# Performance work log

Measured on AMD Instinct MI355X. Metric: run time of the kernel, lower is better.

## Reference

```python
import jax, jax.numpy as jnp
import numpy as np
from jax import lax

NUM_CLASSES = 20
NUM_ANCHORS = 5
COORDS = 4
NMS_TH = 0.45
PRE_TH = 0.005
FEAT_STRIDE = 32.0
BIASES = jnp.array([[1.08, 1.19], [3.42, 4.41], [6.63, 11.38],
                    [9.42, 5.11], [16.62, 10.52]], dtype=jnp.float32)  # [A,2]


def setup_inputs() -> dict:
    key = jax.random.key(0)
    B, H, W = 16, 26, 26
    C = (NUM_CLASSES + COORDS + 1) * NUM_ANCHORS  # 125
    x = jax.random.normal(key, (B, C, H, W), dtype=jnp.float32)
    im_info = jnp.array([480.0, 640.0], dtype=jnp.float32)  # (orig_h, orig_w)
    return {"x": x, "im_info": im_info}


def _pairwise_iou(b):
    # b: [N,4] center-format (cx, cy, w, h)
    x1 = b[:, 0] - b[:, 2] * 0.5
    y1 = b[:, 1] - b[:, 3] * 0.5
    x2 = b[:, 0] + b[:, 2] * 0.5
    y2 = b[:, 1] + b[:, 3] * 0.5
    area = (x2 - x1) * (y2 - y1)
    iw = jnp.maximum(jnp.minimum(x2[:, None], x2[None, :]) - jnp.maximum(x1[:, None], x1[None, :]), 0.0)
    ih = jnp.maximum(jnp.minimum(y2[:, None], y2[None, :]) - jnp.maximum(y1[:, None], y1[None, :]), 0.0)
    inter = iw * ih
    return inter / (area[:, None] + area[None, :] - inter + 1e-12)


def _nms_scores(boxes, scores):
    # greedy single-class NMS; returns scores with pre-threshold + suppressed boxes zeroed
    N = scores.shape[0]
    s = jnp.where(scores < PRE_TH, 0.0, scores)
    order = jnp.argsort(-s)
    ss = s[order]
    iou = lax.stop_gradient(_pairwise_iou(boxes[order]))  # [N,N]
    idx = jnp.arange(N)

    def body(i, keep):
        ki = keep[i] & (ss[i] > 0.0)
        sup = ki & (iou[i] > NMS_TH) & (idx > i)
        return keep & (~sup)

    keep_sorted = lax.fori_loop(0, N, body, jnp.ones((N,), dtype=bool))
    keep = jnp.zeros((N,), dtype=bool).at[order].set(keep_sorted)
    return jnp.where(keep, s, 0.0)


def _forward(x, im_info):
    B, C, H, W = x.shape
    A = NUM_ANCHORS
    fdt = x.dtype

    # --- Slice + activations (channel layout per SLICE_POINTS [10,20,25,125]) ---
    xy = jax.nn.sigmoid(x[:, :2 * A]).reshape(B, A, 2, H, W)
    wh = x[:, 2 * A:4 * A].reshape(B, A, 2, H, W)
    obj = jax.nn.sigmoid(x[:, 4 * A:5 * A])                    # [B,A,H,W]
    conf = x[:, 5 * A:].reshape(B, NUM_CLASSES, A, H, W)

    # --- class probability (plain softmax over class axis 1) + top predictions ---
    class_prob = jax.nn.softmax(conf, axis=1)                  # [B,C,A,H,W]
    top = class_prob * obj[:, None]                            # scale by objectness
    preds = jnp.concatenate([top, obj[:, None]], axis=1)       # [B,C+1,A,H,W]

    # --- YoloBBs: decode boxes on the grid, darknet correct_region_boxes ---
    col = jnp.arange(W, dtype=fdt)[None, None, None, :]
    row = jnp.arange(H, dtype=fdt)[None, None, :, None]
    bx = (col + xy[:, :, 0]) / W                               # [B,A,H,W]
    by = (row + xy[:, :, 1]) / H
    bw = BIASES[None, :, 0, None, None] * jnp.exp(wh[:, :, 0]) / W
    bh = BIASES[None, :, 1, None, None] * jnp.exp(wh[:, :, 1]) / H

    netw = W * FEAT_STRIDE
    neth = H * FEAT_STRIDE
    im_h, im_w = im_info[0], im_info[1]
    cond = (netw / im_w) < (neth / im_h)
    new_w = jnp.where(cond, netw, im_w * neth / im_h)
    new_h = jnp.where(cond, im_h * netw / im_w, neth)
    bx = (bx - (netw - new_w) * 0.5 / netw) / (new_w / netw)
    by = (by - (neth - new_h) * 0.5 / neth) / (new_h / neth)
    bw = bw * (netw / new_w)
    bh = bh * (neth / new_h)
    bboxs = jnp.stack([bx * im_w, by * im_h, bw * im_w, bh * im_h], axis=-1)
    N = A * H * W
    bboxs = bboxs.reshape(B, N, 4)                             # [B,N,4] (cx,cy,w,h) pixels

    # --- NMSFilter (classes=1, first_class=NUM_CLASSES -> objectness channel) ---
    preds_flat = preds.reshape(B, NUM_CLASSES + 1, N)
    obj_scores = preds_flat[:, NUM_CLASSES]                    # [B,N]
    new_obj = jax.vmap(_nms_scores)(bboxs, obj_scores)
    preds_flat = preds_flat.at[:, NUM_CLASSES].set(new_obj)

    # --- YoloEvalCompat: class axis moved last ---
    prob = jnp.transpose(preds_flat, (0, 2, 1))                # [B,N,C+1]
    return prob, bboxs


def reference(x, im_info):
    return _forward(x, im_info)
```

## Files before the change

kernel.cpp:

```cpp
#include <hip/hip_runtime.h>
#include <stdint.h>

#pragma clang fp contract(off)

#define NCLS   20
#define NA     5
#define NB     16
#define Hg     26
#define Wg     26
#define HWc    (Hg*Wg)
#define NBOX   (NA*HWc)
#define NPAD   4096
#define NWRD   (NPAD/64)
#define NROW   3392
#define SWRD   53
#define PROBC  (NCLS+1)
#define PRE_TH 0.005f
#define NMS_TH 0.45f
#define ECHUNK 1024
#define ETOT   88192
#define SEGB(c) (32*(c)*((c)-1))

__constant__ float c_bias[10] = {1.08f,1.19f,3.42f,4.41f,6.63f,11.38f,9.42f,5.11f,16.62f,10.52f};

__global__ __launch_bounds__(256) void k_decode(const float* __restrict__ x,
                                                const float* __restrict__ im_info,
                                                float* __restrict__ out,
                                                float* __restrict__ scores) {
  int t = blockIdx.x * 256 + threadIdx.x;
  if (t >= NB * NBOX) return;
  int b  = t / NBOX;
  int n  = t - b * NBOX;
  int a  = n / HWc;
  int hw = n - a * HWc;
  int h  = hw / Wg;
  int w  = hw - h * Wg;

  const float* xb = x + (size_t)b * 125 * HWc;
  float tx = xb[(2*a  ) * HWc + hw];
  float ty = xb[(2*a+1) * HWc + hw];
  float tw = xb[(10+2*a) * HWc + hw];
  float th = xb[(11+2*a) * HWc + hw];
  float to = xb[(20+a  ) * HWc + hw];

  float sx  = 1.0f / (1.0f + expf(-tx));
  float sy  = 1.0f / (1.0f + expf(-ty));
  float obj = 1.0f / (1.0f + expf(-to));

  float cf[NCLS];
  float mx = -3.402823e38f;
#pragma unroll
  for (int c = 0; c < NCLS; ++c) {
    cf[c] = xb[(25 + c*NA + a) * HWc + hw];
    mx = fmaxf(mx, cf[c]);
  }
  float sum = 0.f;
#pragma unroll
  for (int c = 0; c < NCLS; ++c) { cf[c] = expf(cf[c] - mx); sum += cf[c]; }

  float* op = out + ((size_t)b * NBOX + n) * PROBC;
#pragma unroll
  for (int c = 0; c < NCLS; ++c) op[c] = cf[c] / sum * obj;
  op[NCLS] = 0.f;

  float Wf = (float)Wg, Hf = (float)Hg;
  float bx = ((float)w + sx) / Wf;
  float by = ((float)h + sy) / Hf;
  float bw = c_bias[2*a]   * expf(tw) / Wf;
  float bh = c_bias[2*a+1] * expf(th) / Hf;
  float netw = Wf * 32.0f;
  float neth = Hf * 32.0f;
  float imh = im_info[0], imw = im_info[1];
  bool cond   = (netw / imw) < (neth / imh);
  float new_w = cond ? netw : (imw * neth / imh);
  float new_h = cond ? (imh * netw / imw) : neth;
  bx = (bx - (netw - new_w) * 0.5f / netw) / (new_w / netw);
  by = (by - (neth - new_h) * 0.5f / neth) / (new_h / neth);
  bw = bw * (netw / new_w);
  bh = bh * (neth / new_h);
  float X  = bx * imw, Y = by * imh, Wd = bw * imw, Hd = bh * imh;

  float* ob = out + (size_t)NB * NBOX * PROBC + ((size_t)b * NBOX + n) * 4;
  ob[0] = X; ob[1] = Y; ob[2] = Wd; ob[3] = Hd;

  scores[t] = (obj < PRE_TH) ? 0.f : obj;
}

__global__ __launch_bounds__(1024) void k_sort(const float* __restrict__ scores,
                                               const float* __restrict__ out,
                                               float* __restrict__ sScore,
                                               int* __restrict__ sIdx,
                                               float4* __restrict__ sBox,
                                               unsigned long long* __restrict__ posm,
                                               int* __restrict__ cnt) {
  int b    = blockIdx.x;
  int tid  = threadIdx.x;
  int lane = tid & 63;
  int wv   = tid >> 6;
  __shared__ unsigned long long key[NPAD];

  if (tid < SWRD) cnt[b * SWRD + tid] = 0;

  for (int i = tid; i < NPAD; i += 1024) {
    unsigned long long k = 0ULL;
    if (i < NBOX) {
      float s = scores[b * NBOX + i];
      unsigned int bits = __float_as_uint(s);
      k = ((unsigned long long)bits << 32) | (unsigned long long)(0xFFFFFFFFu - (unsigned)i);
    }
    key[i] = k;
  }
  __syncthreads();

  for (int k = 2; k <= 256; k <<= 1) {
    for (int j = k >> 1; j > 0; j >>= 1) {
#pragma unroll
      for (int qq = 0; qq < 2; ++qq) {
        int q  = lane + (qq << 6);
        int li = ((q & ~(j - 1)) << 1) | (q & (j - 1));
        int i  = (wv << 8) + li;
        int ix = i | j;
        bool desc = ((i & k) == 0);
        unsigned long long a = key[i], c = key[ix];
        bool sw = desc ? (a < c) : (a > c);
        if (sw) { key[i] = c; key[ix] = a; }
      }
      asm volatile("" ::: "memory");
    }
  }
  __syncthreads();

  for (int k = 512; k <= NPAD; k <<= 1) {
    for (int j = k >> 1; j >= 256; j >>= 1) {
#pragma unroll
      for (int qq = 0; qq < 2; ++qq) {
        int q  = tid + (qq << 10);
        int i  = ((q & ~(j - 1)) << 1) | (q & (j - 1));
        int ix = i | j;
        bool desc = ((i & k) == 0);
        unsigned long long a = key[i], c = key[ix];
        bool sw = desc ? (a < c) : (a > c);
        if (sw) { key[i] = c; key[ix] = a; }
      }
      __syncthreads();
    }
    {
      bool desc = (((wv << 8) & k) == 0);
      for (int j = 128; j > 0; j >>= 1) {
#pragma unroll
        for (int qq = 0; qq < 2; ++qq) {
          int q  = lane + (qq << 6);
          int li = ((q & ~(j - 1)) << 1) | (q & (j - 1));
          int i  = (wv << 8) + li;
          int ix = i | j;
          unsigned long long a = key[i], c = key[ix];
          bool sw = desc ? (a < c) : (a > c);
          if (sw) { key[i] = c; key[ix] = a; }
        }
        asm volatile("" ::: "memory");
      }
      __syncthreads();
    }
  }

  const float4* outBox = (const float4*)(out + (size_t)NB * NBOX * PROBC);
  for (int i = tid; i < NPAD; i += 1024) {
    unsigned long long k = key[i];
    float s = __uint_as_float((unsigned)(k >> 32));
    bool pos = (k >> 32) != 0ULL;
    unsigned long long bal = __ballot(pos);
    if ((tid & 63) == 0) posm[b * NWRD + (i >> 6)] = bal;
    sScore[b * NPAD + i] = s;
    int oi = (int)(0xFFFFFFFFu - (unsigned)(k & 0xFFFFFFFFu));
    sIdx[b * NPAD + i] = oi;
    float4 bx = make_float4(0.f, 0.f, 0.f, 0.f);
    if (oi >= 0 && oi < NBOX) bx = outBox[(size_t)b * NBOX + oi];
    sBox[b * NPAD + i] = bx;
  }
}

__global__ __launch_bounds__(64) void k_supmat(const float4* __restrict__ sBox,
                                               unsigned long long* __restrict__ diag,
                                               ulonglong2* __restrict__ entries,
                                               int* __restrict__ cnt) {
  int colg = blockIdx.x;
  int rowg = blockIdx.y;
  if (colg < rowg) return;
  int b = blockIdx.z;
  int l = threadIdx.x;

  __shared__ float4 corn[64];
  __shared__ float  car[64];

  float4 cb = sBox[(size_t)b * NPAD + colg * 64 + l];
  float c1 = cb.x - cb.z * 0.5f;
  float d1 = cb.y - cb.w * 0.5f;
  float c2 = cb.x + cb.z * 0.5f;
  float d2 = cb.y + cb.w * 0.5f;
  corn[l] = make_float4(c1, d1, c2, d2);
  car[l]  = (c2 - c1) * (d2 - d1);
  __syncthreads();

  int row = rowg * 64 + l;
  float4 rb = sBox[(size_t)b * NPAD + row];
  float bx1 = rb.x - rb.z * 0.5f;
  float by1 = rb.y - rb.w * 0.5f;
  float bx2 = rb.x + rb.z * 0.5f;
  float by2 = rb.y + rb.w * 0.5f;
  float areai = (bx2 - bx1) * (by2 - by1);

  int jmin = row - colg * 64;
  unsigned long long bits = 0ULL;
#pragma unroll 4
  for (int t2 = 0; t2 < 64; ++t2) {
    float4 cc = corn[t2];
    float aj  = car[t2];
    float iw = fminf(bx2, cc.z) - fmaxf(bx1, cc.x); iw = fmaxf(iw, 0.0f);
    float ih = fminf(by2, cc.w) - fmaxf(by1, cc.y); ih = fmaxf(ih, 0.0f);
    float inter = iw * ih;
    bool sup = inter > NMS_TH * (areai + aj - inter + 1e-12f);
    if (sup & (t2 > jmin)) bits |= 1ULL << t2;
  }

  if (colg == rowg) {
    diag[((size_t)b * SWRD + colg) * 64 + l] = bits;
  } else if (bits) {
    int p = atomicAdd(&cnt[b * SWRD + colg], 1);
    entries[(size_t)b * ETOT + SEGB(colg) + p] =
        ulonglong2{(unsigned long long)row, bits};
  }
}

__global__ __launch_bounds__(512) void k_scan(const unsigned long long* __restrict__ diag,
                                              const ulonglong2* __restrict__ entries,
                                              const int* __restrict__ cnt,
                                              const unsigned long long* __restrict__ posm,
                                              const float* __restrict__ sScore,
                                              const int* __restrict__ sIdx,
                                              float* __restrict__ out) {
  int b    = blockIdx.x;
  int tid  = threadIdx.x;
  int lane = tid & 63;
  int wid  = tid >> 6;
  __shared__ unsigned long long diagS[SWRD * 64];
  __shared__ ulonglong2 ebuf[2][ECHUNK];
  __shared__ unsigned long long remv[SWRD];
  __shared__ int cntS[SWRD];

  const ulonglong2* segB = entries + (size_t)b * ETOT;

  if (tid < SWRD) {
    remv[tid] = ~posm[b * NWRD + tid];
    cntS[tid] = cnt[b * SWRD + tid];
  }
  for (int i = tid; i < SWRD * 64; i += 512)
    diagS[i] = diag[(size_t)b * SWRD * 64 + i];
  __syncthreads();

  for (int c = 0; c < SWRD; ++c) {
    if (wid > 0) {
      if (c + 1 < SWRD) {
        int nn = cntS[c + 1];
        if (nn > ECHUNK) nn = ECHUNK;
        const ulonglong2* sp = segB + SEGB(c + 1);
        for (int g = tid - 64; g < nn; g += 448) ebuf[(c + 1) & 1][g] = sp[g];
      }
    } else {
      int nc = cntS[c];
      int nl = nc > ECHUNK ? ECHUNK : nc;
      unsigned long long acc = 0ULL;
      for (int g = lane; g < nl; g += 64) {
        ulonglong2 e = ebuf[c & 1][g];
        int row = (int)e.x;
        if (!((remv[row >> 6] >> (row & 63)) & 1ULL)) acc |= e.y;
      }
      for (int g = ECHUNK + lane; g < nc; g += 64) {
        ulonglong2 e = segB[SEGB(c) + g];
        int row = (int)e.x;
        if (!((remv[row >> 6] >> (row & 63)) & 1ULL)) acc |= e.y;
      }
#pragma unroll
      for (int off = 32; off >= 1; off >>= 1) acc |= __shfl_xor(acc, off);

      unsigned long long cur = remv[c] | acc;
      unsigned long long dg  = diagS[(c << 6) + lane];
      unsigned long long m   = __ballot(dg != 0ULL);
      while (m) {
        int k = __ffsll((long long)m) - 1;
        m &= m - 1;
        unsigned long long dk = __shfl(dg, k);
        if (!((cur >> k) & 1ULL)) cur |= dk;
      }
      if (lane == 0) remv[c] = cur;
    }
    __syncthreads();
  }

  for (int p = tid; p < NBOX; p += 512) {
    if (!((remv[p >> 6] >> (p & 63)) & 1ULL)) {
      int oi  = sIdx[b * NPAD + p];
      float s = sScore[b * NPAD + p];
      out[((size_t)b * NBOX + oi) * PROBC + NCLS] = s;
    }
  }
}

extern "C" void kernel_launch(void* const* d_in, const int* in_sizes, int n_in,
                              void* d_out, int out_size, void* d_ws, size_t ws_size,
                              hipStream_t stream) {
  const float* x  = (const float*)d_in[0];
  const float* im = (const float*)d_in[1];
  float* out = (float*)d_out;

  float* scores = (float*)d_ws;
  float* sScore = scores + (size_t)NB * NBOX;
  int*   sIdx   = (int*)(sScore + (size_t)NB * NPAD);
  float4* sBox  = (float4*)(sIdx + (size_t)NB * NPAD);
  unsigned long long* posm = (unsigned long long*)(sBox + (size_t)NB * NPAD);
  unsigned long long* diag = posm + (size_t)NB * NWRD;
  int* cnt = (int*)(diag + (size_t)NB * SWRD * 64);
  ulonglong2* entries = (ulonglong2*)((char*)cnt + (((size_t)NB * SWRD * 4 + 15) & ~(size_t)15));

  hipLaunchKernelGGL(k_decode, dim3((NB * NBOX + 255) / 256), dim3(256), 0, stream,
                     x, im, out, scores);
  hipLaunchKernelGGL(k_sort, dim3(NB), dim3(1024), 0, stream,
                     scores, out, sScore, sIdx, sBox, posm, cnt);
  hipLaunchKernelGGL(k_supmat, dim3(SWRD, SWRD, NB), dim3(64), 0, stream,
                     sBox, diag, entries, cnt);
  hipLaunchKernelGGL(k_scan, dim3(NB), dim3(512), 0, stream,
                     diag, entries, cnt, posm, sScore, sIdx, out);
}
```

Baseline: 209.4 us.

## Preload all suppression entries into LDS once, removing per-column syncs

Measured after the change: 249.1 us. +18.9%, slower.

```diff
diff --git a/kernel.cpp b/kernel.cpp
--- a/kernel.cpp
+++ b/kernel.cpp
@@ -17,9 +17,10 @@
 #define PROBC  (NCLS+1)
 #define PRE_TH 0.005f
 #define NMS_TH 0.45f
-#define ECHUNK 1024
+#define ECAP   8192
 #define ETOT   88192
 #define SEGB(c) (32*(c)*((c)-1))
+#define DYNLDS ((SWRD*64 + ECAP) * 8 + ECAP * 2)
 
 __constant__ float c_bias[10] = {1.08f,1.19f,3.42f,4.41f,6.63f,11.38f,9.42f,5.11f,16.62f,10.52f};
 
@@ -242,42 +243,61 @@
   int tid  = threadIdx.x;
   int lane = tid & 63;
   int wid  = tid >> 6;
-  __shared__ unsigned long long diagS[SWRD * 64];
-  __shared__ ulonglong2 ebuf[2][ECHUNK];
+
+  extern __shared__ char dynS[];
+  unsigned long long* diagS = (unsigned long long*)dynS;
+  unsigned long long* bitsS = diagS + SWRD * 64;
+  unsigned short*     rowS  = (unsigned short*)(bitsS + ECAP);
   __shared__ unsigned long long remv[SWRD];
-  __shared__ int cntS[SWRD];
+  __shared__ int offs[SWRD + 1];
 
   const ulonglong2* segB = entries + (size_t)b * ETOT;
 
-  if (tid < SWRD) {
-    remv[tid] = ~posm[b * NWRD + tid];
-    cntS[tid] = cnt[b * SWRD + tid];
-  }
+  if (tid < SWRD) remv[tid] = ~posm[b * NWRD + tid];
   for (int i = tid; i < SWRD * 64; i += 512)
     diagS[i] = diag[(size_t)b * SWRD * 64 + i];
-  __syncthreads();
-
-  for (int c = 0; c < SWRD; ++c) {
-    if (wid > 0) {
-      if (c + 1 < SWRD) {
-        int nn = cntS[c + 1];
-        if (nn > ECHUNK) nn = ECHUNK;
-        const ulonglong2* sp = segB + SEGB(c + 1);
-        for (int g = tid - 64; g < nn; g += 448) ebuf[(c + 1) & 1][g] = sp[g];
-      }
-    } else {
-      int nc = cntS[c];
-      int nl = nc > ECHUNK ? ECHUNK : nc;
+
+  if (wid == 0) {
+    int v = (lane < SWRD) ? cnt[b * SWRD + lane] : 0;
+    int s = v;
+#pragma unroll
+    for (int d = 1; d < 64; d <<= 1) {
+      int o = __shfl_up(s, d);
+      if (lane >= d) s += o;
+    }
+    if (lane < SWRD) offs[lane + 1] = s;
+    if (lane == 0)  offs[0] = 0;
+  }
+  __syncthreads();
+
+  int total = offs[SWRD];
+  bool inLds = (total <= ECAP);
+  if (inLds) {
+    for (int g = tid; g < total; g += 512) {
+      int lo = 0, hi = SWRD;
+      while (hi - lo > 1) { int mid = (lo + hi) >> 1; if (offs[mid] <= g) lo = mid; else hi = mid; }
+      ulonglong2 e = segB[SEGB(lo) + (g - offs[lo])];
+      bitsS[g] = e.y;
+      rowS[g]  = (unsigned short)e.x;
+    }
+  }
+  __syncthreads();
+
+  if (wid == 0) {
+    for (int c = 0; c < SWRD; ++c) {
+      int e0 = offs[c], e1 = offs[c + 1];
       unsigned long long acc = 0ULL;
-      for (int g = lane; g < nl; g += 64) {
-        ulonglong2 e = ebuf[c & 1][g];
-        int row = (int)e.x;
-        if (!((remv[row >> 6] >> (row & 63)) & 1ULL)) acc |= e.y;
-      }
-      for (int g = ECHUNK + lane; g < nc; g += 64) {
-        ulonglong2 e = segB[SEGB(c) + g];
-        int row = (int)e.x;
-        if (!((remv[row >> 6] >> (row & 63)) & 1ULL)) acc |= e.y;
+      if (inLds) {
+        for (int g = e0 + lane; g < e1; g += 64) {
+          int row = rowS[g];
+          if (!((remv[row >> 6] >> (row & 63)) & 1ULL)) acc |= bitsS[g];
+        }
+      } else {
+        for (int g = e0 + lane; g < e1; g += 64) {
+          ulonglong2 e = segB[SEGB(c) + (g - e0)];
+          int row = (int)e.x;
+          if (!((remv[row >> 6] >> (row & 63)) & 1ULL)) acc |= e.y;
+        }
       }
 #pragma unroll
       for (int off = 32; off >= 1; off >>= 1) acc |= __shfl_xor(acc, off);
@@ -293,8 +313,8 @@
       }
       if (lane == 0) remv[c] = cur;
     }
-    __syncthreads();
-  }
+  }
+  __syncthreads();
 
   for (int p = tid; p < NBOX; p += 512) {
     if (!((remv[p >> 6] >> (p & 63)) & 1ULL)) {
@@ -321,12 +341,19 @@
   int* cnt = (int*)(diag + (size_t)NB * SWRD * 64);
   ulonglong2* entries = (ulonglong2*)((char*)cnt + (((size_t)NB * SWRD * 4 + 15) & ~(size_t)15));
 
+  static bool attrSet = false;
+  if (!attrSet) {
+    hipFuncSetAttribute((const void*)k_scan,
+                        hipFuncAttributeMaxDynamicSharedMemorySize, DYNLDS);
+    attrSet = true;
+  }
+
   hipLaunchKernelGGL(k_decode, dim3((NB * NBOX + 255) / 256), dim3(256), 0, stream,
                      x, im, out, scores);
   hipLaunchKernelGGL(k_sort, dim3(NB), dim3(1024), 0, stream,
                      scores, out, sScore, sIdx, sBox, posm, cnt);
   hipLaunchKernelGGL(k_supmat, dim3(SWRD, SWRD, NB), dim3(64), 0, stream,
                      sBox, diag, entries, cnt);
-  hipLaunchKernelGGL(k_scan, dim3(NB), dim3(512), 0, stream,
+  hipLaunchKernelGGL(k_scan, dim3(NB), dim3(512), DYNLDS, stream,
                      diag, entries, cnt, posm, sScore, sIdx, out);
 }
```
